# Optimization experiments

Measured on AMD Instinct MI355X. Metric: run time of the kernel, lower is better.

Reference implementation:

```python
import jax, jax.numpy as jnp
import numpy as np

N, E, H, C = 10000, 160000, 7, 64
NEG_SLOPE = 0.2


def setup_inputs() -> dict:
    key = jax.random.key(0)
    ks = iter(jax.random.split(key, 32))
    def w(shape, fan_in):
        return jax.random.normal(next(ks), shape, jnp.float32) * (1.0 / np.sqrt(fan_in))
    inp = {
        "x": jax.random.normal(next(ks), (N, 1024), jnp.float32),
        "edge_index": jax.random.randint(next(ks), (2, E), 0, N, jnp.int64),
        # input MLP 1024->512->256->64
        "W1": w((1024, 512), 1024), "b1": jnp.zeros((512,), jnp.float32),
        "W2": w((512, 256), 512),   "b2": jnp.zeros((256,), jnp.float32),
        "W3": w((256, 64), 256),    "b3": jnp.zeros((64,), jnp.float32),
        # 5 stacked GATv2Conv(64,64,heads=7,concat=False) layers
        "Wl": w((5, 64, H * C), 64), "bl": jnp.zeros((5, H * C), jnp.float32),
        "Wr": w((5, 64, H * C), 64),
        "att": w((5, H, C), C),
        "cbias": jnp.zeros((5, C), jnp.float32),
        # output MLP 64->32->16->9
        "V1": w((64, 32), 64), "c1": jnp.zeros((32,), jnp.float32),
        "V2": w((32, 16), 32), "c2": jnp.zeros((16,), jnp.float32),
        "V3": w((16, 9), 16),  "c3": jnp.zeros((9,), jnp.float32),
    }
    return inp


def _gatv2_conv(x, src, dst, Wl, bl, Wr, att, bias):
    # x: [N,64]; src/dst: [E'] (self-loops already appended)
    xl = (x @ Wl + bl).reshape(N, H, C)   # lin_l (with bias)
    xr = (x @ Wr).reshape(N, H, C)        # lin_r (no bias)
    e = jax.nn.leaky_relu(xl[src] + xr[dst], NEG_SLOPE)      # [E',H,C]
    logits = jnp.einsum('ehc,hc->eh', e, att)                # [E',H]
    m = jax.ops.segment_max(logits, dst, num_segments=N)     # [N,H]
    a = jnp.exp(logits - m[dst])
    s = jax.ops.segment_sum(a, dst, num_segments=N)          # [N,H]
    alpha = a / (s[dst] + 1e-16)                             # ragged softmax per dst node
    out = jax.ops.segment_sum(alpha[:, :, None] * xl[src], dst, num_segments=N)  # [N,H,C]
    return out.mean(axis=1) + bias                           # concat=False -> mean heads


def reference(x, edge_index, W1, b1, W2, b2, W3, b3, Wl, bl, Wr, att, cbias,
              V1, c1, V2, c2, V3, c3):
    # GATv2Conv adds self-loops by default
    loops = jnp.arange(N, dtype=edge_index.dtype)
    src = jnp.concatenate([edge_index[0], loops])
    dst = jnp.concatenate([edge_index[1], loops])

    h = jax.nn.relu(x @ W1 + b1)
    h = jax.nn.relu(h @ W2 + b2)
    h = jax.nn.relu(h @ W3 + b3)
    for l in range(5):
        h = jax.nn.relu(_gatv2_conv(h, src, dst, Wl[l], bl[l], Wr[l], att[l], cbias[l]))
    h = jax.nn.relu(h) @ V1 + c1
    h = jax.nn.relu(h) @ V2 + c2
    h = jax.nn.relu(h) @ V3 + c3
    return jax.nn.log_softmax(h, axis=1)
```

## Files before the change

### kernel.cpp

```cpp
#include <hip/hip_runtime.h>
#include <hip/hip_bf16.h>
#include <math.h>

#define NNODES 10000
#define NEDGES 160000
#define ETOT (NEDGES + NNODES)
#define HEADS 7
#define CH 64
#define HC 448
#define HCP 1024

typedef __attribute__((ext_vector_type(8))) short short8;
typedef __attribute__((ext_vector_type(4))) float floatx4;

__device__ __forceinline__ float bf_lo(unsigned u) {
  return __uint_as_float(u << 16);
}
__device__ __forceinline__ float bf_hi(unsigned u) {
  return __uint_as_float(u & 0xffff0000u);
}
__device__ __forceinline__ short f2bf(float v) {
  return __bfloat16_as_short(__float2bfloat16(v));
}

#define P0 2560000
#define P1 (P0 + 512 * 1024)
#define P2 (P1 + 256 * 512)
#define P3 (P2 + 64 * 256)
#define P4 (P3 + 5 * HCP * 64)
#define P5 (P4 + 5 * HCP)
#define P6 (P5 + NNODES)
#define PTOT P6

__global__ __launch_bounds__(256) void prep_kernel(
    const float* __restrict__ x, short* __restrict__ xb,
    const float* __restrict__ W1, short* __restrict__ W1t,
    const float* __restrict__ W2, short* __restrict__ W2t,
    const float* __restrict__ W3, short* __restrict__ W3t,
    const float* __restrict__ Wl, const float* __restrict__ Wr,
    const float* __restrict__ bl, short* __restrict__ Wgt,
    float* __restrict__ bg, int* __restrict__ cnt) {
  int idx = blockIdx.x * 256 + threadIdx.x;
  if (idx < P0) {
    float4 v = *(const float4*)&x[(size_t)idx * 4];
    short4 o;
    o.x = f2bf(v.x); o.y = f2bf(v.y); o.z = f2bf(v.z); o.w = f2bf(v.w);
    *(short4*)&xb[(size_t)idx * 4] = o;
  } else if (idx < P1) {
    int i = idx - P0;
    int n = i / 1024, k = i % 1024;
    W1t[i] = f2bf(W1[(size_t)k * 512 + n]);
  } else if (idx < P2) {
    int i = idx - P1;
    int n = i / 512, k = i % 512;
    W2t[i] = f2bf(W2[(size_t)k * 256 + n]);
  } else if (idx < P3) {
    int i = idx - P2;
    int n = i / 256, k = i % 256;
    W3t[i] = f2bf(W3[(size_t)k * 64 + n]);
  } else if (idx < P4) {
    int i = idx - P3;
    int l = i / (HCP * 64);
    int rem = i % (HCP * 64);
    int col = rem / 64, k = rem % 64;
    int half = col >> 9;
    int within = col & 511;
    int c = within >> 3, h = within & 7;
    float v = 0.f;
    if (h < 7) {
      const float* W = half ? Wr : Wl;
      v = W[((size_t)l * 64 + k) * HC + h * 64 + c];
    }
    Wgt[i] = f2bf(v);
  } else if (idx < P5) {
    int i = idx - P4;
    int l = i >> 10, col = i & 1023;
    int half = col >> 9, within = col & 511;
    int c = within >> 3, h = within & 7;
    bg[i] = (!half && h < 7) ? bl[(size_t)l * HC + h * 64 + c] : 0.f;
  } else if (idx < P6) {
    cnt[idx - P5] = 1;
  }
}

template <int BM, int BN, int RELU>
__global__ __launch_bounds__(256) void mfma_gemm(
    const short* __restrict__ A, const short* __restrict__ Bt,
    const float* __restrict__ bias, short* __restrict__ C,
    int M, int K, int Nc) {
  __shared__ short As[BM * 64];
  __shared__ short Bs[BN * 64];
  constexpr int MI = BM / 32;
  constexpr int NJ = BN / 32;
  int tid = threadIdx.x;
  int lane = tid & 63, wave = tid >> 6;
  int wm = wave >> 1, wn = wave & 1;
  int row0 = blockIdx.x * BM, col0 = blockIdx.y * BN;
  floatx4 acc[MI][NJ] = {};

  for (int k0 = 0; k0 < K; k0 += 64) {
    #pragma unroll
    for (int i = 0; i < BM / 32; ++i) {
      int c = i * 4 + wave;
      int r = c * 8 + (lane >> 3);
      int k = (lane & 7) * 8;
      int grow = row0 + r;
      if (grow >= M) grow = M - 1;
      __builtin_amdgcn_global_load_lds(
          (const __attribute__((address_space(1))) void*)(A + (size_t)grow * K + k0 + k),
          (__attribute__((address_space(3))) void*)(As + c * 512), 16, 0, 0);
    }
    #pragma unroll
    for (int i = 0; i < BN / 32; ++i) {
      int c = i * 4 + wave;
      int r = c * 8 + (lane >> 3);
      int k = (lane & 7) * 8;
      int gcol = col0 + r;
      if (gcol >= Nc) gcol = Nc - 1;
      __builtin_amdgcn_global_load_lds(
          (const __attribute__((address_space(1))) void*)(Bt + (size_t)gcol * K + k0 + k),
          (__attribute__((address_space(3))) void*)(Bs + c * 512), 16, 0, 0);
    }
    __syncthreads();
    int lr = lane & 15, lq = lane >> 4;
    #pragma unroll
    for (int kk = 0; kk < 64; kk += 32) {
      short8 af[MI], bf[NJ];
      #pragma unroll
      for (int i = 0; i < MI; ++i)
        af[i] = *(const short8*)&As[(wm * (BM / 2) + i * 16 + lr) * 64 + kk + lq * 8];
      #pragma unroll
      for (int j = 0; j < NJ; ++j)
        bf[j] = *(const short8*)&Bs[(wn * (BN / 2) + j * 16 + lr) * 64 + kk + lq * 8];
      #pragma unroll
      for (int i = 0; i < MI; ++i)
        #pragma unroll
        for (int j = 0; j < NJ; ++j)
          acc[i][j] = __builtin_amdgcn_mfma_f32_16x16x32_bf16(
              af[i], bf[j], acc[i][j], 0, 0, 0);
    }
    __syncthreads();
  }

  int lr = lane & 15, lq = lane >> 4;
  #pragma unroll
  for (int j = 0; j < NJ; ++j) {
    int col = col0 + wn * (BN / 2) + j * 16 + lr;
    float bj = bias ? bias[col] : 0.f;
    #pragma unroll
    for (int i = 0; i < MI; ++i) {
      int rbase = row0 + wm * (BM / 2) + i * 16 + lq * 4;
      #pragma unroll
      for (int r = 0; r < 4; ++r) {
        int row = rbase + r;
        if (row < M) {
          float v = acc[i][j][r] + bj;
          if (RELU) v = fmaxf(v, 0.f);
          C[(size_t)row * Nc + col] = f2bf(v);
        }
      }
    }
  }
}

__global__ void hist_kernel(const int* __restrict__ ei, int* __restrict__ cnt) {
  int e = blockIdx.x * 256 + threadIdx.x;
  if (e < NEDGES) atomicAdd(&cnt[ei[NEDGES + e]], 1);
}

__global__ __launch_bounds__(1024) void scan_kernel(
    const int* __restrict__ cnt, int* __restrict__ row_start,
    int* __restrict__ cursor) {
  __shared__ int wsum[16];
  int t = threadIdx.x;
  int lane = t & 63, w = t >> 6;
  int base = t * 10;
  int v[10], s = 0;
  #pragma unroll
  for (int i = 0; i < 10; ++i) {
    v[i] = (base + i < NNODES) ? cnt[base + i] : 0;
    s += v[i];
  }
  int incl = s;
  #pragma unroll
  for (int off = 1; off < 64; off <<= 1) {
    int o = __shfl_up(incl, off, 64);
    if (lane >= off) incl += o;
  }
  if (lane == 63) wsum[w] = incl;
  __syncthreads();
  if (w == 0) {
    int wv = (lane < 16) ? wsum[lane] : 0;
    #pragma unroll
    for (int off = 1; off < 16; off <<= 1) {
      int o = __shfl_up(wv, off, 64);
      if (lane >= off) wv += o;
    }
    if (lane < 16) wsum[lane] = wv;
  }
  __syncthreads();
  int woff = (w > 0) ? wsum[w - 1] : 0;
  int excl = woff + incl - s;
  #pragma unroll
  for (int i = 0; i < 10; ++i) {
    if (base + i < NNODES) {
      row_start[base + i] = excl;
      cursor[base + i] = excl;
    }
    excl += v[i];
  }
  if (t == 1023) row_start[NNODES] = wsum[15];
}

__global__ void scatter_kernel(const int* __restrict__ ei,
                               int* __restrict__ cursor,
                               int* __restrict__ csr_src,
                               int* __restrict__ csr_dst) {
  int t = blockIdx.x * 256 + threadIdx.x;
  if (t < NNODES) {
    int pos = atomicAdd(&cursor[t], 1);
    csr_src[pos] = t;
    csr_dst[pos] = t;
  } else if (t < ETOT) {
    int e = t - NNODES;
    int d = ei[NEDGES + e];
    int pos = atomicAdd(&cursor[d], 1);
    csr_src[pos] = ei[e];
    csr_dst[pos] = d;
  }
}

__global__ __launch_bounds__(256) void edge_logits_kernel(
    const short* __restrict__ xlt, const float* __restrict__ att,
    const int* __restrict__ csr_src, const int* __restrict__ csr_dst,
    float* __restrict__ wbuf) {
  __shared__ float att_s[512];
  for (int i = threadIdx.x; i < 512; i += 256) {
    int c = i >> 3, h = i & 7;
    att_s[i] = (h < 7) ? att[h * 64 + c] : 0.f;
  }
  __syncthreads();
  int lane = threadIdx.x & 63;
  int wid = threadIdx.x >> 6;
  int eo = lane >> 3, cl = lane & 7;
  int base = (blockIdx.x * 4 + wid) * 16;
  int e0 = base + eo;
  int e1 = base + 8 + eo;
  int ec0 = (e0 < ETOT) ? e0 : (ETOT - 1);
  int ec1 = (e1 < ETOT) ? e1 : (ETOT - 1);
  int sA = csr_src[ec0], dA = csr_dst[ec0];
  int sB = csr_src[ec1], dB = csr_dst[ec1];
  const uint4* xlpA = (const uint4*)(xlt + (size_t)sA * HCP);
  const uint4* xrpA = (const uint4*)(xlt + (size_t)dA * HCP + 512);
  const uint4* xlpB = (const uint4*)(xlt + (size_t)sB * HCP);
  const uint4* xrpB = (const uint4*)(xlt + (size_t)dB * HCP + 512);
  float accA[7], accB[7];
  #pragma unroll
  for (int h = 0; h < 7; ++h) { accA[h] = 0.f; accB[h] = 0.f; }
  #pragma unroll
  for (int q = 0; q < 8; ++q) {
    int c = q * 8 + cl;
    uint4 aA = xlpA[c];
    uint4 bA = xrpA[c];
    uint4 aB = xlpB[c];
    uint4 bB = xrpB[c];
    float4 t0 = *(const float4*)&att_s[c * 8];
    float4 t1 = *(const float4*)&att_s[c * 8 + 4];
    {
      float e0v = bf_lo(aA.x) + bf_lo(bA.x);
      float e1v = bf_hi(aA.x) + bf_hi(bA.x);
      float e2v = bf_lo(aA.y) + bf_lo(bA.y);
      float e3v = bf_hi(aA.y) + bf_hi(bA.y);
      float e4v = bf_lo(aA.z) + bf_lo(bA.z);
      float e5v = bf_hi(aA.z) + bf_hi(bA.z);
      float e6v = bf_lo(aA.w) + bf_lo(bA.w);
      e0v = fmaxf(e0v, 0.2f * e0v); e1v = fmaxf(e1v, 0.2f * e1v);
      e2v = fmaxf(e2v, 0.2f * e2v); e3v = fmaxf(e3v, 0.2f * e3v);
      e4v = fmaxf(e4v, 0.2f * e4v); e5v = fmaxf(e5v, 0.2f * e5v);
      e6v = fmaxf(e6v, 0.2f * e6v);
      accA[0] += t0.x * e0v; accA[1] += t0.y * e1v;
      accA[2] += t0.z * e2v; accA[3] += t0.w * e3v;
      accA[4] += t1.x * e4v; accA[5] += t1.y * e5v;
      accA[6] += t1.z * e6v;
    }
    {
      float e0v = bf_lo(aB.x) + bf_lo(bB.x);
      float e1v = bf_hi(aB.x) + bf_hi(bB.x);
      float e2v = bf_lo(aB.y) + bf_lo(bB.y);
      float e3v = bf_hi(aB.y) + bf_hi(bB.y);
      float e4v = bf_lo(aB.z) + bf_lo(bB.z);
      float e5v = bf_hi(aB.z) + bf_hi(bB.z);
      float e6v = bf_lo(aB.w) + bf_lo(bB.w);
      e0v = fmaxf(e0v, 0.2f * e0v); e1v = fmaxf(e1v, 0.2f * e1v);
      e2v = fmaxf(e2v, 0.2f * e2v); e3v = fmaxf(e3v, 0.2f * e3v);
      e4v = fmaxf(e4v, 0.2f * e4v); e5v = fmaxf(e5v, 0.2f * e5v);
      e6v = fmaxf(e6v, 0.2f * e6v);
      accB[0] += t0.x * e0v; accB[1] += t0.y * e1v;
      accB[2] += t0.z * e2v; accB[3] += t0.w * e3v;
      accB[4] += t1.x * e4v; accB[5] += t1.y * e5v;
      accB[6] += t1.z * e6v;
    }
  }
  #pragma unroll
  for (int h = 0; h < 7; ++h) {
    accA[h] += __shfl_xor(accA[h], 1, 64);
    accA[h] += __shfl_xor(accA[h], 2, 64);
    accA[h] += __shfl_xor(accA[h], 4, 64);
    accB[h] += __shfl_xor(accB[h], 1, 64);
    accB[h] += __shfl_xor(accB[h], 2, 64);
    accB[h] += __shfl_xor(accB[h], 4, 64);
  }
  float resA = 0.f, resB = 0.f;
  #pragma unroll
  for (int h = 0; h < 7; ++h) {
    resA = (cl == h) ? accA[h] : resA;
    resB = (cl == h) ? accB[h] : resB;
  }
  float wA = (cl < 7) ? __expf(resA) : 0.f;
  float wB = (cl < 7) ? __expf(resB) : 0.f;
  if (e0 < ETOT) wbuf[(size_t)e0 * 8 + cl] = wA;
  if (e1 < ETOT) wbuf[(size_t)e1 * 8 + cl] = wB;
}

template <int FINAL>
__global__ __launch_bounds__(256) void gat_agg2_kernel(
    const short* __restrict__ xlt, const float* __restrict__ wbuf,
    const float* __restrict__ cbias, const int* __restrict__ row_start,
    const int* __restrict__ csr_src, short* __restrict__ hout,
    const float* __restrict__ V1, const float* __restrict__ c1,
    const float* __restrict__ V2, const float* __restrict__ c2,
    const float* __restrict__ V3, const float* __restrict__ c3,
    float* __restrict__ out) {
  __shared__ float part[2][14][64];
  __shared__ float hb[2][64], r1[2][32], r2[2][16], z3[2][9];
  int lane = threadIdx.x & 63;
  int wv = threadIdx.x >> 6;
  int nw = wv >> 1;
  int half = wv & 1;
  int n = blockIdx.x * 2 + nw;
  int beg = row_start[n], end = row_start[n + 1];

  float o0 = 0.f, o1 = 0.f, o2 = 0.f, o3 = 0.f, o4 = 0.f, o5 = 0.f, o6 = 0.f;
  float s0 = 0.f, s1 = 0.f, s2 = 0.f, s3 = 0.f, s4 = 0.f, s5 = 0.f, s6 = 0.f;
  #pragma unroll 4
  for (int e = beg + half; e < end; e += 2) {
    int src = csr_src[e];
    float4 wa = *(const float4*)&wbuf[(size_t)e * 8];
    float4 wb = *(const float4*)&wbuf[(size_t)e * 8 + 4];
    uint4 xv = *(const uint4*)(xlt + (size_t)src * HCP + (size_t)lane * 8);
    o0 += wa.x * bf_lo(xv.x);
    o1 += wa.y * bf_hi(xv.x);
    o2 += wa.z * bf_lo(xv.y);
    o3 += wa.w * bf_hi(xv.y);
    o4 += wb.x * bf_lo(xv.z);
    o5 += wb.y * bf_hi(xv.z);
    o6 += wb.z * bf_lo(xv.w);
    s0 += wa.x; s1 += wa.y; s2 += wa.z; s3 += wa.w;
    s4 += wb.x; s5 += wb.y; s6 += wb.z;
  }

  if (half == 1) {
    part[nw][0][lane] = o0;  part[nw][1][lane] = o1;
    part[nw][2][lane] = o2;  part[nw][3][lane] = o3;
    part[nw][4][lane] = o4;  part[nw][5][lane] = o5;
    part[nw][6][lane] = o6;
    part[nw][7][lane] = s0;  part[nw][8][lane] = s1;
    part[nw][9][lane] = s2;  part[nw][10][lane] = s3;
    part[nw][11][lane] = s4; part[nw][12][lane] = s5;
    part[nw][13][lane] = s6;
  }
  __syncthreads();
  if (half == 0) {
    o0 += part[nw][0][lane];  o1 += part[nw][1][lane];
    o2 += part[nw][2][lane];  o3 += part[nw][3][lane];
    o4 += part[nw][4][lane];  o5 += part[nw][5][lane];
    o6 += part[nw][6][lane];
    s0 += part[nw][7][lane];  s1 += part[nw][8][lane];
    s2 += part[nw][9][lane];  s3 += part[nw][10][lane];
    s4 += part[nw][11][lane]; s5 += part[nw][12][lane];
    s6 += part[nw][13][lane];
    float accv = o0 / (s0 + 1e-16f) + o1 / (s1 + 1e-16f) + o2 / (s2 + 1e-16f) +
                 o3 / (s3 + 1e-16f) + o4 / (s4 + 1e-16f) + o5 / (s5 + 1e-16f) +
                 o6 / (s6 + 1e-16f);
    float v = fmaxf(accv * (1.0f / 7.0f) + cbias[lane], 0.f);
    if (!FINAL) {
      hout[(size_t)n * 64 + lane] = f2bf(v);
    } else {
      int t = lane;
      hb[nw][t] = v;
      if (t < 32) {
        float a = c1[t];
        #pragma unroll
        for (int k = 0; k < 64; ++k) a += hb[nw][k] * V1[k * 32 + t];
        r1[nw][t] = fmaxf(a, 0.f);
      }
      if (t < 16) {
        float a = c2[t];
        #pragma unroll
        for (int k = 0; k < 32; ++k) a += r1[nw][k] * V2[k * 16 + t];
        r2[nw][t] = fmaxf(a, 0.f);
      }
      if (t < 9) {
        float a = c3[t];
        #pragma unroll
        for (int k = 0; k < 16; ++k) a += r2[nw][k] * V3[k * 9 + t];
        z3[nw][t] = a;
      }
      if (t < 9) {
        float mx = z3[nw][0];
        #pragma unroll
        for (int k = 1; k < 9; ++k) mx = fmaxf(mx, z3[nw][k]);
        float s = 0.f;
        #pragma unroll
        for (int k = 0; k < 9; ++k) s += __expf(z3[nw][k] - mx);
        out[(size_t)n * 9 + t] = z3[nw][t] - mx - logf(s);
      }
    }
  }
}

extern "C" void kernel_launch(void* const* d_in, const int* in_sizes, int n_in,
                              void* d_out, int out_size, void* d_ws, size_t ws_size,
                              hipStream_t stream) {
  const float* x   = (const float*)d_in[0];
  const int*   ei  = (const int*)d_in[1];
  const float* W1  = (const float*)d_in[2];
  const float* b1  = (const float*)d_in[3];
  const float* W2  = (const float*)d_in[4];
  const float* b2  = (const float*)d_in[5];
  const float* W3  = (const float*)d_in[6];
  const float* b3  = (const float*)d_in[7];
  const float* Wl  = (const float*)d_in[8];
  const float* bl  = (const float*)d_in[9];
  const float* Wr  = (const float*)d_in[10];
  const float* att = (const float*)d_in[11];
  const float* cb  = (const float*)d_in[12];
  const float* V1  = (const float*)d_in[13];
  const float* c1  = (const float*)d_in[14];
  const float* V2  = (const float*)d_in[15];
  const float* c2  = (const float*)d_in[16];
  const float* V3  = (const float*)d_in[17];
  const float* c3  = (const float*)d_in[18];
  float* out = (float*)d_out;

  char* ws = (char*)d_ws;
  size_t off = 0;
  auto alloc = [&](size_t bytes) {
    void* p = ws + off;
    off = (off + bytes + 255) & ~(size_t)255;
    return p;
  };
  char* region0 = (char*)alloc((size_t)NNODES * 1024 * 2 + 1024);
  short* xb  = (short*)region0;
  short* h2  = (short*)region0;
  short* xlt = (short*)region0;
  char* region1 = (char*)alloc((size_t)NNODES * 512 * 2 + 1024);
  short* h1 = (short*)region1;
  short* hA = (short*)region1;
  short* hB = hA + (size_t)NNODES * 64;
  short* W1t = (short*)alloc((size_t)512 * 1024 * 2);
  short* W2t = (short*)alloc((size_t)256 * 512 * 2);
  short* W3t = (short*)alloc((size_t)64 * 256 * 2);
  short* Wgt = (short*)alloc((size_t)5 * HCP * 64 * 2);
  float* bg  = (float*)alloc((size_t)5 * HCP * 4);
  int* cnt       = (int*)alloc((size_t)NNODES * 4);
  int* row_start = (int*)alloc((size_t)(NNODES + 1) * 4);
  int* cursor    = (int*)alloc((size_t)NNODES * 4);
  int* csr_src   = (int*)alloc((size_t)ETOT * 4);
  int* csr_dst   = (int*)alloc((size_t)ETOT * 4);
  float* wbuf    = (float*)alloc((size_t)ETOT * 8 * 4);

  prep_kernel<<<(PTOT + 255) / 256, 256, 0, stream>>>(
      x, xb, W1, W1t, W2, W2t, W3, W3t, Wl, Wr, bl, Wgt, bg, cnt);

  hist_kernel<<<(NEDGES + 255) / 256, 256, 0, stream>>>(ei, cnt);
  scan_kernel<<<1, 1024, 0, stream>>>(cnt, row_start, cursor);
  scatter_kernel<<<(ETOT + 255) / 256, 256, 0, stream>>>(ei, cursor, csr_src, csr_dst);

  mfma_gemm<64, 128, 1><<<dim3(157, 4), 256, 0, stream>>>(
      xb, W1t, b1, h1, NNODES, 1024, 512);
  mfma_gemm<64, 128, 1><<<dim3(157, 2), 256, 0, stream>>>(
      h1, W2t, b2, h2, NNODES, 512, 256);
  mfma_gemm<64, 64, 1><<<dim3(157, 1), 256, 0, stream>>>(
      h2, W3t, b3, hA, NNODES, 256, 64);

  short* hcur = hA;
  short* hnext = hB;
  for (int layer = 0; layer < 5; ++layer) {
    mfma_gemm<128, 128, 0><<<dim3(79, 8), 256, 0, stream>>>(
        hcur, Wgt + (size_t)layer * HCP * 64, bg + (size_t)layer * HCP, xlt,
        NNODES, 64, HCP);
    edge_logits_kernel<<<(ETOT + 63) / 64, 256, 0, stream>>>(
        xlt, att + (size_t)layer * HC, csr_src, csr_dst, wbuf);
    if (layer < 4) {
      gat_agg2_kernel<0><<<5000, 256, 0, stream>>>(
          xlt, wbuf, cb + (size_t)layer * 64, row_start, csr_src, hnext,
          V1, c1, V2, c2, V3, c3, out);
    } else {
      gat_agg2_kernel<1><<<5000, 256, 0, stream>>>(
          xlt, wbuf, cb + (size_t)layer * 64, row_start, csr_src, hnext,
          V1, c1, V2, c2, V3, c3, out);
    }
    short* tmp = hcur; hcur = hnext; hnext = tmp;
  }
}
```

Baseline: 551.5 us.

## Fuse edge-logit computation into per-node GAT aggregation kernel

Removes the separate edge_logits kernel and its wbuf round trip. Each aggregation wave now computes exp-logits for 8 incoming edges at a time and stages the weights and source indices in LDS, then accumulates them. The dst projection row is loaded once per node, and csr_dst is no longer needed. In exchange, the per-node loop is serialised into compute-then-aggregate phases, and low-degree nodes leave lanes idle in the logit phase.

```diff
diff --git a/kernel.cpp b/kernel.cpp
--- a/kernel.cpp
+++ b/kernel.cpp
@@ -214,149 +214,117 @@
 
 __global__ void scatter_kernel(const int* __restrict__ ei,
                                int* __restrict__ cursor,
-                               int* __restrict__ csr_src,
-                               int* __restrict__ csr_dst) {
+                               int* __restrict__ csr_src) {
   int t = blockIdx.x * 256 + threadIdx.x;
   if (t < NNODES) {
     int pos = atomicAdd(&cursor[t], 1);
     csr_src[pos] = t;
-    csr_dst[pos] = t;
   } else if (t < ETOT) {
     int e = t - NNODES;
     int d = ei[NEDGES + e];
     int pos = atomicAdd(&cursor[d], 1);
     csr_src[pos] = ei[e];
-    csr_dst[pos] = d;
-  }
-}
-
-__global__ __launch_bounds__(256) void edge_logits_kernel(
+  }
+}
+
+template <int FINAL>
+__global__ __launch_bounds__(256) void gat_fused_kernel(
     const short* __restrict__ xlt, const float* __restrict__ att,
-    const int* __restrict__ csr_src, const int* __restrict__ csr_dst,
-    float* __restrict__ wbuf) {
-  __shared__ float att_s[512];
-  for (int i = threadIdx.x; i < 512; i += 256) {
-    int c = i >> 3, h = i & 7;
-    att_s[i] = (h < 7) ? att[h * 64 + c] : 0.f;
-  }
-  __syncthreads();
-  int lane = threadIdx.x & 63;
-  int wid = threadIdx.x >> 6;
-  int eo = lane >> 3, cl = lane & 7;
-  int base = (blockIdx.x * 4 + wid) * 16;
-  int e0 = base + eo;
-  int e1 = base + 8 + eo;
-  int ec0 = (e0 < ETOT) ? e0 : (ETOT - 1);
-  int ec1 = (e1 < ETOT) ? e1 : (ETOT - 1);
-  int sA = csr_src[ec0], dA = csr_dst[ec0];
-  int sB = csr_src[ec1], dB = csr_dst[ec1];
-  const uint4* xlpA = (const uint4*)(xlt + (size_t)sA * HCP);
-  const uint4* xrpA = (const uint4*)(xlt + (size_t)dA * HCP + 512);
-  const uint4* xlpB = (const uint4*)(xlt + (size_t)sB * HCP);
-  const uint4* xrpB = (const uint4*)(xlt + (size_t)dB * HCP + 512);
-  float accA[7], accB[7];
-  #pragma unroll
-  for (int h = 0; h < 7; ++h) { accA[h] = 0.f; accB[h] = 0.f; }
-  #pragma unroll
-  for (int q = 0; q < 8; ++q) {
-    int c = q * 8 + cl;
-    uint4 aA = xlpA[c];
-    uint4 bA = xrpA[c];
-    uint4 aB = xlpB[c];
-    uint4 bB = xrpB[c];
-    float4 t0 = *(const float4*)&att_s[c * 8];
-    float4 t1 = *(const float4*)&att_s[c * 8 + 4];
-    {
-      float e0v = bf_lo(aA.x) + bf_lo(bA.x);
-      float e1v = bf_hi(aA.x) + bf_hi(bA.x);
-      float e2v = bf_lo(aA.y) + bf_lo(bA.y);
-      float e3v = bf_hi(aA.y) + bf_hi(bA.y);
-      float e4v = bf_lo(aA.z) + bf_lo(bA.z);
-      float e5v = bf_hi(aA.z) + bf_hi(bA.z);
-      float e6v = bf_lo(aA.w) + bf_lo(bA.w);
-      e0v = fmaxf(e0v, 0.2f * e0v); e1v = fmaxf(e1v, 0.2f * e1v);
-      e2v = fmaxf(e2v, 0.2f * e2v); e3v = fmaxf(e3v, 0.2f * e3v);
-      e4v = fmaxf(e4v, 0.2f * e4v); e5v = fmaxf(e5v, 0.2f * e5v);
-      e6v = fmaxf(e6v, 0.2f * e6v);
-      accA[0] += t0.x * e0v; accA[1] += t0.y * e1v;
-      accA[2] += t0.z * e2v; accA[3] += t0.w * e3v;
-      accA[4] += t1.x * e4v; accA[5] += t1.y * e5v;
-      accA[6] += t1.z * e6v;
-    }
-    {
-      float e0v = bf_lo(aB.x) + bf_lo(bB.x);
-      float e1v = bf_hi(aB.x) + bf_hi(bB.x);
-      float e2v = bf_lo(aB.y) + bf_lo(bB.y);
-      float e3v = bf_hi(aB.y) + bf_hi(bB.y);
-      float e4v = bf_lo(aB.z) + bf_lo(bB.z);
-      float e5v = bf_hi(aB.z) + bf_hi(bB.z);
-      float e6v = bf_lo(aB.w) + bf_lo(bB.w);
-      e0v = fmaxf(e0v, 0.2f * e0v); e1v = fmaxf(e1v, 0.2f * e1v);
-      e2v = fmaxf(e2v, 0.2f * e2v); e3v = fmaxf(e3v, 0.2f * e3v);
-      e4v = fmaxf(e4v, 0.2f * e4v); e5v = fmaxf(e5v, 0.2f * e5v);
-      e6v = fmaxf(e6v, 0.2f * e6v);
-      accB[0] += t0.x * e0v; accB[1] += t0.y * e1v;
-      accB[2] += t0.z * e2v; accB[3] += t0.w * e3v;
-      accB[4] += t1.x * e4v; accB[5] += t1.y * e5v;
-      accB[6] += t1.z * e6v;
-    }
-  }
-  #pragma unroll
-  for (int h = 0; h < 7; ++h) {
-    accA[h] += __shfl_xor(accA[h], 1, 64);
-    accA[h] += __shfl_xor(accA[h], 2, 64);
-    accA[h] += __shfl_xor(accA[h], 4, 64);
-    accB[h] += __shfl_xor(accB[h], 1, 64);
-    accB[h] += __shfl_xor(accB[h], 2, 64);
-    accB[h] += __shfl_xor(accB[h], 4, 64);
-  }
-  float resA = 0.f, resB = 0.f;
-  #pragma unroll
-  for (int h = 0; h < 7; ++h) {
-    resA = (cl == h) ? accA[h] : resA;
-    resB = (cl == h) ? accB[h] : resB;
-  }
-  float wA = (cl < 7) ? __expf(resA) : 0.f;
-  float wB = (cl < 7) ? __expf(resB) : 0.f;
-  if (e0 < ETOT) wbuf[(size_t)e0 * 8 + cl] = wA;
-  if (e1 < ETOT) wbuf[(size_t)e1 * 8 + cl] = wB;
-}
-
-template <int FINAL>
-__global__ __launch_bounds__(256) void gat_agg2_kernel(
-    const short* __restrict__ xlt, const float* __restrict__ wbuf,
     const float* __restrict__ cbias, const int* __restrict__ row_start,
     const int* __restrict__ csr_src, short* __restrict__ hout,
     const float* __restrict__ V1, const float* __restrict__ c1,
     const float* __restrict__ V2, const float* __restrict__ c2,
     const float* __restrict__ V3, const float* __restrict__ c3,
     float* __restrict__ out) {
+  __shared__ float att_s[512];
   __shared__ float part[2][14][64];
+  __shared__ float wlds[4][8][8];
+  __shared__ int   slds[4][8];
   __shared__ float hb[2][64], r1[2][32], r2[2][16], z3[2][9];
+
+  for (int i = threadIdx.x; i < 512; i += 256) {
+    int c = i >> 3, h = i & 7;
+    att_s[i] = (h < 7) ? att[h * 64 + c] : 0.f;
+  }
+  __syncthreads();
+
   int lane = threadIdx.x & 63;
   int wv = threadIdx.x >> 6;
   int nw = wv >> 1;
   int half = wv & 1;
   int n = blockIdx.x * 2 + nw;
   int beg = row_start[n], end = row_start[n + 1];
+  int t0c = end - beg - half;
+  int cnt = (t0c > 0) ? ((t0c + 1) >> 1) : 0;
+
+  int le = lane >> 3, cl = lane & 7;
+  const uint4* xrp = (const uint4*)(xlt + (size_t)n * HCP + 512);
 
   float o0 = 0.f, o1 = 0.f, o2 = 0.f, o3 = 0.f, o4 = 0.f, o5 = 0.f, o6 = 0.f;
   float s0 = 0.f, s1 = 0.f, s2 = 0.f, s3 = 0.f, s4 = 0.f, s5 = 0.f, s6 = 0.f;
-  #pragma unroll 4
-  for (int e = beg + half; e < end; e += 2) {
+
+  for (int i0 = 0; i0 < cnt; i0 += 8) {
+    int idx = i0 + le;
+    int ide = (idx < cnt) ? idx : (cnt - 1);
+    int e = beg + half + 2 * ide;
     int src = csr_src[e];
-    float4 wa = *(const float4*)&wbuf[(size_t)e * 8];
-    float4 wb = *(const float4*)&wbuf[(size_t)e * 8 + 4];
-    uint4 xv = *(const uint4*)(xlt + (size_t)src * HCP + (size_t)lane * 8);
-    o0 += wa.x * bf_lo(xv.x);
-    o1 += wa.y * bf_hi(xv.x);
-    o2 += wa.z * bf_lo(xv.y);
-    o3 += wa.w * bf_hi(xv.y);
-    o4 += wb.x * bf_lo(xv.z);
-    o5 += wb.y * bf_hi(xv.z);
-    o6 += wb.z * bf_lo(xv.w);
-    s0 += wa.x; s1 += wa.y; s2 += wa.z; s3 += wa.w;
-    s4 += wb.x; s5 += wb.y; s6 += wb.z;
+    if (cl == 0) slds[wv][le] = src;
+    const uint4* xlp = (const uint4*)(xlt + (size_t)src * HCP);
+    float acc[7] = {0.f, 0.f, 0.f, 0.f, 0.f, 0.f, 0.f};
+    #pragma unroll
+    for (int q = 0; q < 8; ++q) {
+      int c = q * 8 + cl;
+      uint4 a = xlp[c];
+      uint4 b = xrp[c];
+      float4 t0 = *(const float4*)&att_s[c * 8];
+      float4 t1 = *(const float4*)&att_s[c * 8 + 4];
+      float e0v = bf_lo(a.x) + bf_lo(b.x);
+      float e1v = bf_hi(a.x) + bf_hi(b.x);
+      float e2v = bf_lo(a.y) + bf_lo(b.y);
+      float e3v = bf_hi(a.y) + bf_hi(b.y);
+      float e4v = bf_lo(a.z) + bf_lo(b.z);
+      float e5v = bf_hi(a.z) + bf_hi(b.z);
+      float e6v = bf_lo(a.w) + bf_lo(b.w);
+      e0v = fmaxf(e0v, 0.2f * e0v); e1v = fmaxf(e1v, 0.2f * e1v);
+      e2v = fmaxf(e2v, 0.2f * e2v); e3v = fmaxf(e3v, 0.2f * e3v);
+      e4v = fmaxf(e4v, 0.2f * e4v); e5v = fmaxf(e5v, 0.2f * e5v);
+      e6v = fmaxf(e6v, 0.2f * e6v);
+      acc[0] += t0.x * e0v; acc[1] += t0.y * e1v;
+      acc[2] += t0.z * e2v; acc[3] += t0.w * e3v;
+      acc[4] += t1.x * e4v; acc[5] += t1.y * e5v;
+      acc[6] += t1.z * e6v;
+    }
+    #pragma unroll
+    for (int h = 0; h < 7; ++h) {
+      acc[h] += __shfl_xor(acc[h], 1, 64);
+      acc[h] += __shfl_xor(acc[h], 2, 64);
+      acc[h] += __shfl_xor(acc[h], 4, 64);
+    }
+    float res = 0.f;
+    #pragma unroll
+    for (int h = 0; h < 7; ++h) res = (cl == h) ? acc[h] : res;
+    wlds[wv][le][cl] = (cl < 7) ? __expf(res) : 0.f;
+    asm volatile("" ::: "memory");
+
+    int m = cnt - i0;
+    if (m > 8) m = 8;
+    #pragma unroll 4
+    for (int j = 0; j < m; ++j) {
+      int src2 = slds[wv][j];
+      float4 wa = *(const float4*)&wlds[wv][j][0];
+      float4 wb = *(const float4*)&wlds[wv][j][4];
+      uint4 xv = *(const uint4*)(xlt + (size_t)src2 * HCP + (size_t)lane * 8);
+      o0 += wa.x * bf_lo(xv.x);
+      o1 += wa.y * bf_hi(xv.x);
+      o2 += wa.z * bf_lo(xv.y);
+      o3 += wa.w * bf_hi(xv.y);
+      o4 += wb.x * bf_lo(xv.z);
+      o5 += wb.y * bf_hi(xv.z);
+      o6 += wb.z * bf_lo(xv.w);
+      s0 += wa.x; s1 += wa.y; s2 += wa.z; s3 += wa.w;
+      s4 += wb.x; s5 += wb.y; s6 += wb.z;
+    }
+    asm volatile("" ::: "memory");
   }
 
   if (half == 1) {
@@ -467,15 +435,13 @@
   int* row_start = (int*)alloc((size_t)(NNODES + 1) * 4);
   int* cursor    = (int*)alloc((size_t)NNODES * 4);
   int* csr_src   = (int*)alloc((size_t)ETOT * 4);
-  int* csr_dst   = (int*)alloc((size_t)ETOT * 4);
-  float* wbuf    = (float*)alloc((size_t)ETOT * 8 * 4);
 
   prep_kernel<<<(PTOT + 255) / 256, 256, 0, stream>>>(
       x, xb, W1, W1t, W2, W2t, W3, W3t, Wl, Wr, bl, Wgt, bg, cnt);
 
   hist_kernel<<<(NEDGES + 255) / 256, 256, 0, stream>>>(ei, cnt);
   scan_kernel<<<1, 1024, 0, stream>>>(cnt, row_start, cursor);
-  scatter_kernel<<<(ETOT + 255) / 256, 256, 0, stream>>>(ei, cursor, csr_src, csr_dst);
+  scatter_kernel<<<(ETOT + 255) / 256, 256, 0, stream>>>(ei, cursor, csr_src);
 
   mfma_gemm<64, 128, 1><<<dim3(157, 4), 256, 0, stream>>>(
       xb, W1t, b1, h1, NNODES, 1024, 512);
@@ -490,16 +456,14 @@
     mfma_gemm<128, 128, 0><<<dim3(79, 8), 256, 0, stream>>>(
         hcur, Wgt + (size_t)layer * HCP * 64, bg + (size_t)layer * HCP, xlt,
         NNODES, 64, HCP);
-    edge_logits_kernel<<<(ETOT + 63) / 64, 256, 0, stream>>>(
-        xlt, att + (size_t)layer * HC, csr_src, csr_dst, wbuf);
     if (layer < 4) {
-      gat_agg2_kernel<0><<<5000, 256, 0, stream>>>(
-          xlt, wbuf, cb + (size_t)layer * 64, row_start, csr_src, hnext,
-          V1, c1, V2, c2, V3, c3, out);
+      gat_fused_kernel<0><<<5000, 256, 0, stream>>>(
+          xlt, att + (size_t)layer * HC, cb + (size_t)layer * 64, row_start,
+          csr_src, hnext, V1, c1, V2, c2, V3, c3, out);
     } else {
-      gat_agg2_kernel<1><<<5000, 256, 0, stream>>>(
-          xlt, wbuf, cb + (size_t)layer * 64, row_start, csr_src, hnext,
-          V1, c1, V2, c2, V3, c3, out);
+      gat_fused_kernel<1><<<5000, 256, 0, stream>>>(
+          xlt, att + (size_t)layer * HC, cb + (size_t)layer * 64, row_start,
+          csr_src, hnext, V1, c1, V2, c2, V3, c3, out);
     }
     short* tmp = hcur; hcur = hnext; hnext = tmp;
   }
```

New measurement: 579.9 us. 5.2% more time.
